# Kernel optimization log

Hardware: AMD Instinct MI355X
Metric: run time of the kernel (lower is better)

## Reference

```python
import jax, jax.numpy as jnp
import numpy as np

# Mesh/element sizes (cubic-Lagrange-like triangle element: 3 vertex + 6 edge + 1 face dofs)
C = 500_000   # num cells
V = 250_000   # num vertices
E = 750_000   # num edges
DV = 1        # dofs per vertex
DE = 2        # dofs per edge
DF = 1        # dofs per face
Q = 16        # quadrature points per cell
NB = 3 * DV + 3 * DE + DF  # = 10 basis functions per cell


def setup_inputs() -> dict:
    key = jax.random.key(0)
    ks = jax.random.split(key, 7)
    vertex_dofs = jax.random.normal(ks[0], (V, DV), dtype=jnp.float32)
    edge_dofs = jax.random.normal(ks[1], (E, DE), dtype=jnp.float32)
    face_dofs = jax.random.normal(ks[2], (C, DF), dtype=jnp.float32)
    y = jax.random.normal(ks[3], (C, NB, Q), dtype=jnp.float32)
    faces = jax.random.randint(ks[4], (C, 3), 0, V)
    faces_to_edges = jax.random.randint(ks[5], (C, 3), 0, E)
    edge_orientation = jax.random.randint(ks[6], (C, 3), 0, 2)
    return {
        "vertex_dofs": vertex_dofs,
        "edge_dofs": edge_dofs,
        "face_dofs": face_dofs,
        "y": y,
        "faces": faces,
        "faces_to_edges": faces_to_edges,
        "edge_orientation": edge_orientation,
    }


def reference(vertex_dofs, edge_dofs, face_dofs, y, faces, faces_to_edges, edge_orientation):
    # Gather vertex dofs per cell: [C, 3, DV] -> [C, 3*DV]
    local_vertex = vertex_dofs[faces].reshape(faces.shape[0], -1)

    # Gather edge dofs per cell: [C, 3, DE]
    local_edge = edge_dofs[faces_to_edges]
    o = edge_orientation[:, :, None].astype(local_edge.dtype)  # [C, 3, 1]
    # Flip dof order along the edge when orientation == 0
    local_edge = local_edge * o + jnp.flip(local_edge, axis=2) * (1.0 - o)
    local_edge = local_edge.reshape(local_edge.shape[0], -1)  # [C, 3*DE]

    # Concatenate all local dofs: [C, NB]
    local_dofs = jnp.concatenate([local_vertex, local_edge, face_dofs], axis=1)

    # Weighted sum over basis functions: sum_b local_dofs[c,b] * y[c,b,q] -> [C, Q]
    return jnp.einsum('cb,cbq->cq', local_dofs, y)
```

## Files before the change

kernel.cpp:

```cpp
#include <hip/hip_runtime.h>


#define NBASIS 10

__global__ __launch_bounds__(256) void quad_kernel(
    const float*  __restrict__ vertex_dofs,
    const float*  __restrict__ edge_dofs,
    const float*  __restrict__ face_dofs,
    const float4* __restrict__ y4,
    const int*    __restrict__ faces,
    const int*    __restrict__ f2e,
    const int*    __restrict__ orient,
    float4*       __restrict__ out4,
    int C)
{
    int t = blockIdx.x * blockDim.x + threadIdx.x;
    int c = t >> 2;
    if (c >= C) return;
    int l = t & 3;

    float ld[NBASIS];

    #pragma unroll
    for (int j = 0; j < 3; ++j) {
        ld[j] = vertex_dofs[faces[3 * c + j]];
    }

    #pragma unroll
    for (int j = 0; j < 3; ++j) {
        int e = f2e[3 * c + j];
        int o = orient[3 * c + j];
        float e0 = edge_dofs[2 * e + 0];
        float e1 = edge_dofs[2 * e + 1];
        ld[3 + 2 * j + 0] = o ? e0 : e1;
        ld[3 + 2 * j + 1] = o ? e1 : e0;
    }

    ld[9] = face_dofs[c];

    const float4* yp = y4 + (size_t)c * 40 + l;
    float4 acc = make_float4(0.f, 0.f, 0.f, 0.f);
    #pragma unroll
    for (int b = 0; b < NBASIS; ++b) {
        float4 v = yp[(size_t)b * 4];
        acc.x = fmaf(ld[b], v.x, acc.x);
        acc.y = fmaf(ld[b], v.y, acc.y);
        acc.z = fmaf(ld[b], v.z, acc.z);
        acc.w = fmaf(ld[b], v.w, acc.w);
    }

    out4[(size_t)c * 4 + l] = acc;
}

extern "C" void kernel_launch(void* const* d_in, const int* in_sizes, int n_in,
                              void* d_out, int out_size, void* d_ws, size_t ws_size,
                              hipStream_t stream) {
    const float*  vertex_dofs = (const float*)d_in[0];
    const float*  edge_dofs   = (const float*)d_in[1];
    const float*  face_dofs   = (const float*)d_in[2];
    const float4* y4          = (const float4*)d_in[3];
    const int*    faces       = (const int*)d_in[4];
    const int*    f2e         = (const int*)d_in[5];
    const int*    orient      = (const int*)d_in[6];
    float4*       out4        = (float4*)d_out;

    const int C = in_sizes[2];
    const int threads = C * 4;
    const int block = 256;
    const int grid = (threads + block - 1) / block;

    quad_kernel<<<grid, block, 0, stream>>>(vertex_dofs, edge_dofs, face_dofs,
                                            y4, faces, f2e, orient, out4, C);
}
```

Before: 450.7 us.

## Split per-cell dof gathers across the 4 lanes via shared memory and prefetch y

Before, each of the 4 threads serving a cell redundantly gathered all 10 local dofs. Now each lane gathers only a subset (vertices, or one edge plus the face dof), writes it to shared memory, and the block synchronizes before the weighted sum. All 10 y float4 loads are issued before the gathers so their latency overlaps the dependent index loads. The cost is a block barrier, shared memory use, and extra registers to hold the prefetched y values.

```diff
diff --git a/kernel.cpp b/kernel.cpp
--- a/kernel.cpp
+++ b/kernel.cpp
@@ -2,6 +2,8 @@
 
 
 #define NBASIS 10
+#define CPB 64
+#define LDSTRIDE 12
 
 __global__ __launch_bounds__(256) void quad_kernel(
     const float*  __restrict__ vertex_dofs,
@@ -14,42 +16,56 @@
     float4*       __restrict__ out4,
     int C)
 {
-    int t = blockIdx.x * blockDim.x + threadIdx.x;
-    int c = t >> 2;
-    if (c >= C) return;
-    int l = t & 3;
+    __shared__ float sld[CPB * LDSTRIDE];
 
-    float ld[NBASIS];
+    const int tid   = threadIdx.x;
+    const int lcell = tid >> 2;
+    const int part  = tid & 3;
+    const int c     = blockIdx.x * CPB + lcell;
+    const bool valid = (c < C);
 
-    #pragma unroll
-    for (int j = 0; j < 3; ++j) {
-        ld[j] = vertex_dofs[faces[3 * c + j]];
+    float4 v[NBASIS];
+    if (valid) {
+        const float4* yp = y4 + (size_t)c * (NBASIS * 4) + part;
+        #pragma unroll
+        for (int b = 0; b < NBASIS; ++b) {
+            v[b] = yp[(size_t)b * 4];
+        }
+
+        float* ld = &sld[lcell * LDSTRIDE];
+        if (part == 0) {
+            int f0 = faces[3 * c + 0];
+            int f1 = faces[3 * c + 1];
+            int f2 = faces[3 * c + 2];
+            ld[0] = vertex_dofs[f0];
+            ld[1] = vertex_dofs[f1];
+            ld[2] = vertex_dofs[f2];
+        } else {
+            const int j = part - 1;
+            int e = f2e[3 * c + j];
+            int o = orient[3 * c + j];
+            float2 ev = ((const float2*)edge_dofs)[e];
+            ld[3 + 2 * j + 0] = o ? ev.x : ev.y;
+            ld[3 + 2 * j + 1] = o ? ev.y : ev.x;
+            if (part == 1) ld[9] = face_dofs[c];
+        }
     }
 
-    #pragma unroll
-    for (int j = 0; j < 3; ++j) {
-        int e = f2e[3 * c + j];
-        int o = orient[3 * c + j];
-        float e0 = edge_dofs[2 * e + 0];
-        float e1 = edge_dofs[2 * e + 1];
-        ld[3 + 2 * j + 0] = o ? e0 : e1;
-        ld[3 + 2 * j + 1] = o ? e1 : e0;
+    __syncthreads();
+
+    if (valid) {
+        const float* ld = &sld[lcell * LDSTRIDE];
+        float4 acc = make_float4(0.f, 0.f, 0.f, 0.f);
+        #pragma unroll
+        for (int b = 0; b < NBASIS; ++b) {
+            float w = ld[b];
+            acc.x = fmaf(w, v[b].x, acc.x);
+            acc.y = fmaf(w, v[b].y, acc.y);
+            acc.z = fmaf(w, v[b].z, acc.z);
+            acc.w = fmaf(w, v[b].w, acc.w);
+        }
+        out4[(size_t)c * 4 + part] = acc;
     }
-
-    ld[9] = face_dofs[c];
-
-    const float4* yp = y4 + (size_t)c * 40 + l;
-    float4 acc = make_float4(0.f, 0.f, 0.f, 0.f);
-    #pragma unroll
-    for (int b = 0; b < NBASIS; ++b) {
-        float4 v = yp[(size_t)b * 4];
-        acc.x = fmaf(ld[b], v.x, acc.x);
-        acc.y = fmaf(ld[b], v.y, acc.y);
-        acc.z = fmaf(ld[b], v.z, acc.z);
-        acc.w = fmaf(ld[b], v.w, acc.w);
-    }
-
-    out4[(size_t)c * 4 + l] = acc;
 }
 
 extern "C" void kernel_launch(void* const* d_in, const int* in_sizes, int n_in,
@@ -65,10 +81,8 @@
     float4*       out4        = (float4*)d_out;
 
     const int C = in_sizes[2];
-    const int threads = C * 4;
-    const int block = 256;
-    const int grid = (threads + block - 1) / block;
+    const int grid = (C + CPB - 1) / CPB;
 
-    quad_kernel<<<grid, block, 0, stream>>>(vertex_dofs, edge_dofs, face_dofs,
-                                            y4, faces, f2e, orient, out4, C);
+    quad_kernel<<<grid, 256, 0, stream>>>(vertex_dofs, edge_dofs, face_dofs,
+                                          y4, faces, f2e, orient, out4, C);
 }
```

Measured after the change: 454.7 us. About the same (+0.9%).
